# Kernel tuning notes

Measured on AMD Instinct MI355X. Metric: run time of the kernel, lower is better.

## Reference

```python
import jax, jax.numpy as jnp
import numpy as np

# Fixed varlen layout: 2 sequences of length 2048 packed into N=4096 tokens
B, S, H, HK, D = 2, 2048, 32, 8, 128
G = H // HK  # GQA group size
SCALE = 1.0 / float(np.sqrt(D))


def setup_inputs() -> dict:
    key = jax.random.key(0)
    k0, k1, k2 = jax.random.split(key, 3)
    N = B * S
    return {
        "q": jax.random.normal(k0, (N, H, D), jnp.float32),
        "k": jax.random.normal(k1, (N, HK, D), jnp.float32),
        "v": jax.random.normal(k2, (N, HK, D), jnp.float32),
        "k_cache": jnp.zeros((N, HK * D), jnp.float32),
        "v_cache": jnp.zeros((N, HK * D), jnp.float32),
        "slot_mapping": jnp.arange(N, dtype=jnp.int32),
    }


def reference(q, k, v, k_cache, v_cache, slot_mapping):
    N = q.shape[0]
    num_slots = k_cache.shape[0]
    # --- store_kvcache: scatter flattened K/V rows into paged slots; slot==-1 skipped ---
    safe = jnp.where(slot_mapping >= 0, slot_mapping, num_slots)  # out-of-range -> dropped
    k_cache_new = k_cache.at[safe].set(k.reshape(N, HK * D), mode="drop")
    v_cache_new = v_cache.at[safe].set(v.reshape(N, HK * D), mode="drop")
    # --- prefill path (block_tables=None): causal varlen attention on fresh k,v ---
    qb = q.reshape(B, S, HK, G, D)
    kb = k.reshape(B, S, HK, D)
    vb = v.reshape(B, S, HK, D)
    scores = jnp.einsum("bqhgd,bkhd->bhgqk", qb, kb) * SCALE  # [B,HK,G,S,S]
    causal = jnp.tril(jnp.ones((S, S), dtype=bool))
    scores = jnp.where(causal, scores, jnp.finfo(scores.dtype).min)
    p = jax.nn.softmax(scores, axis=-1)
    o = jnp.einsum("bhgqk,bkhd->bqhgd", p, vb).reshape(N, H, D)
    return o, k_cache_new, v_cache_new
```

## Files before the change

kernel.cpp:

```cpp
#include <hip/hip_runtime.h>
#include <stdint.h>
#include <math.h>

constexpr int B = 2, S = 2048, H = 32, HK = 8, D = 128;
constexpr int N = B * S;
constexpr int KVD = HK * D;
constexpr float SCALE = 0.08838834764831845f;
constexpr float LOG2E = 1.4426950408889634f;
constexpr float QSCALE = SCALE * LOG2E;

typedef __attribute__((ext_vector_type(8))) short short8;
typedef __attribute__((ext_vector_type(4))) float floatx4;

static __device__ __forceinline__ uint32_t f2bf1(float f) {
    union { float f; uint32_t u; } c; c.f = f;
    return (c.u + 0x7FFFu + ((c.u >> 16) & 1u)) >> 16;
}
static __device__ __forceinline__ uint32_t packbf(float a, float b) {
    return f2bf1(a) | (f2bf1(b) << 16);
}
static __device__ __forceinline__ uint32_t fbits(float f) {
    union { float f; uint32_t u; } c; c.f = f; return c.u;
}
static __device__ __forceinline__ uint32_t packtrunc(float lo, float hi) {
    return __builtin_amdgcn_perm(fbits(hi), fbits(lo), 0x07060302u);
}
static __device__ __forceinline__ void load_lds16(const void* g, void* l) {
    __builtin_amdgcn_global_load_lds((const __attribute__((address_space(1))) uint32_t*)g,
                                     (__attribute__((address_space(3))) uint32_t*)l,
                                     16, 0, 0);
}

__global__ __launch_bounds__(256) void k_prep(const float* __restrict__ k,
                                              const int* __restrict__ slot_mapping,
                                              float* __restrict__ kc_out,
                                              uint16_t* __restrict__ Kb) {
    int tid = blockIdx.x * 256 + threadIdx.x;
    int idx = tid * 4;
    int token = idx >> 10;
    int rem = idx & 1023;
    float4 val = *(const float4*)(k + idx);
    int s = slot_mapping[token];
    if (s >= 0 && s < N) {
        *(float4*)(kc_out + (size_t)s * KVD + rem) = val;
    }
    int b  = token >> 11;
    int ss = token & 2047;
    int hk = rem >> 7;
    int d  = rem & 127;
    uint2 pk;
    pk.x = packbf(val.x, val.y);
    pk.y = packbf(val.z, val.w);
    *(uint2*)(Kb + (((size_t)(b * HK + hk) * S + ss) * D + d)) = pk;
}

__global__ __launch_bounds__(256) void v_prep(const float* __restrict__ v,
                                              const int* __restrict__ slot_mapping,
                                              float* __restrict__ vc_out,
                                              uint16_t* __restrict__ Vt) {
    __shared__ float tile[64][129];
    int t = threadIdx.x;
    int kv0 = blockIdx.x * 64;
    int bhk = blockIdx.y;
    int b = bhk >> 3, hk = bhk & 7;

#pragma unroll
    for (int i = 0; i < 8; ++i) {
        int r = i * 8 + (t >> 5);
        int c = (t & 31) * 4;
        int token = b * S + kv0 + r;
        float4 val = *(const float4*)(v + (size_t)token * KVD + hk * D + c);
        int s = slot_mapping[token];
        if (s >= 0 && s < N) {
            *(float4*)(vc_out + (size_t)s * KVD + hk * D + c) = val;
        }
        tile[r][c + 0] = val.x; tile[r][c + 1] = val.y;
        tile[r][c + 2] = val.z; tile[r][c + 3] = val.w;
    }
    __syncthreads();
#pragma unroll
    for (int i = 0; i < 8; ++i) {
        int d = i * 16 + (t >> 4);
        int c = (t & 15) * 4;
        uint2 pk;
        pk.x = packbf(tile[c + 0][d], tile[c + 1][d]);
        pk.y = packbf(tile[c + 2][d], tile[c + 3][d]);
        *(uint2*)(Vt + ((size_t)(bhk * D + d)) * S + kv0 + c) = pk;
    }
}

__global__ __launch_bounds__(512, 2) void attn(const float* __restrict__ q,
                                               const uint16_t* __restrict__ Kb,
                                               const uint16_t* __restrict__ Vt,
                                               float* __restrict__ out) {
    __shared__ uint16_t sK[2][64 * 128];
    __shared__ uint16_t sV[2][128 * 64];

    int id = blockIdx.x;
    int hk = id & 7;
    int s0 = id >> 3;
    int x  = s0 & 7;
    int g2 = (s0 >> 3) & 1;
    int b  = s0 >> 4;
    int h0 = hk * 4 + g2 * 2;

    int t = threadIdx.x;
    int lane = t & 63, wave = t >> 6;
    int quad = lane >> 4, n = lane & 15, xr = n & 7;

    const uint16_t* Kbh = Kb + (size_t)(b * HK + hk) * S * D;
    const uint16_t* Vbh = Vt + (size_t)(b * HK + hk) * D * S;

    const uint16_t* gK[2]; const uint16_t* gV[2];
    int oK[2], oV[2];
#pragma unroll
    for (int j = 0; j < 2; ++j) {
        int i = wave * 2 + j;
        int rK = i * 4 + (lane >> 4);
        int cK = ((lane & 15) ^ (rK & 7)) * 8;
        gK[j] = Kbh + (size_t)rK * D + cK;
        oK[j] = i * 512;
        int rV = i * 8 + (lane >> 3);
        int cV = ((lane & 7) ^ (rV & 7)) * 8;
        gV[j] = Vbh + (size_t)rV * S + cV;
        oV[j] = i * 512;
    }

    for (int pass = 0; pass < 2; ++pass) {
        int qt = pass ? x : 15 - x;
        int q0 = qt * 128;
        int qwave = q0 + wave * 16;

        short8 bq[2][4];
#pragma unroll
        for (int g = 0; g < 2; ++g) {
            const float* qrow = q + (size_t)(b * S + qwave + n) * (H * D) + (h0 + g) * D + quad * 8;
#pragma unroll
            for (int kc = 0; kc < 4; ++kc) {
                float4 v0 = *(const float4*)(qrow + kc * 32);
                float4 v1 = *(const float4*)(qrow + kc * 32 + 4);
                uint4 pk;
                pk.x = packtrunc(v0.x * QSCALE, v0.y * QSCALE);
                pk.y = packtrunc(v0.z * QSCALE, v0.w * QSCALE);
                pk.z = packtrunc(v1.x * QSCALE, v1.y * QSCALE);
                pk.w = packtrunc(v1.z * QSCALE, v1.w * QSCALE);
                bq[g][kc] = *(short8*)&pk;
            }
        }

        floatx4 o_acc[2][8];
#pragma unroll
        for (int g = 0; g < 2; ++g)
#pragma unroll
            for (int i = 0; i < 8; ++i) o_acc[g][i] = (floatx4){0.f, 0.f, 0.f, 0.f};
        float lsum[2] = {0.f, 0.f};

        int nt = 2 * qt + 2;
        __syncthreads();
#pragma unroll
        for (int j = 0; j < 2; ++j) load_lds16(gK[j], &sK[0][0] + oK[j]);
#pragma unroll
        for (int j = 0; j < 2; ++j) load_lds16(gV[j], &sV[0][0] + oV[j]);

        for (int tile = 0; tile < nt; ++tile) {
            int cur = tile & 1;
            __syncthreads();
            if (tile + 1 < nt) {
                int kvn = (tile + 1) * 64;
#pragma unroll
                for (int j = 0; j < 2; ++j) load_lds16(gK[j] + (size_t)kvn * D, &sK[cur ^ 1][0] + oK[j]);
#pragma unroll
                for (int j = 0; j < 2; ++j) load_lds16(gV[j] + kvn, &sV[cur ^ 1][0] + oV[j]);
            }
            int kv0 = tile * 64;
            if (kv0 > qwave + 15) continue;

            const uint16_t* K_ = &sK[cur][0];
            const uint16_t* V_ = &sV[cur][0];

            floatx4 acc[2][4];
#pragma unroll
            for (int g = 0; g < 2; ++g)
#pragma unroll
                for (int sub = 0; sub < 4; ++sub) acc[g][sub] = (floatx4){0.f, 0.f, 0.f, 0.f};
#pragma unroll
            for (int sub = 0; sub < 4; ++sub) {
#pragma unroll
                for (int kc = 0; kc < 4; ++kc) {
                    short8 ak = *(const short8*)(K_ + (sub * 16 + n) * 128 + (((kc * 4 + quad) ^ xr) * 8));
                    acc[0][sub] = __builtin_amdgcn_mfma_f32_16x16x32_bf16(ak, bq[0][kc], acc[0][sub], 0, 0, 0);
                    acc[1][sub] = __builtin_amdgcn_mfma_f32_16x16x32_bf16(ak, bq[1][kc], acc[1][sub], 0, 0, 0);
                }
            }

            short8 ap[2][2];
            int qg = qwave + n;
            if (kv0 + 63 > qwave) {
#pragma unroll
                for (int sub = 0; sub < 4; ++sub)
#pragma unroll
                    for (int reg = 0; reg < 4; ++reg)
                        if (kv0 + sub * 16 + quad * 4 + reg > qg) {
                            acc[0][sub][reg] = -1e9f;
                            acc[1][sub][reg] = -1e9f;
                        }
            }
#pragma unroll
            for (int g = 0; g < 2; ++g) {
                float rs = 0.f;
                uint32_t pw[4][2];
#pragma unroll
                for (int sub = 0; sub < 4; ++sub) {
                    float p0 = __builtin_amdgcn_exp2f(acc[g][sub][0]);
                    float p1 = __builtin_amdgcn_exp2f(acc[g][sub][1]);
                    float p2 = __builtin_amdgcn_exp2f(acc[g][sub][2]);
                    float p3 = __builtin_amdgcn_exp2f(acc[g][sub][3]);
                    rs += (p0 + p1) + (p2 + p3);
                    pw[sub][0] = packtrunc(p0, p1);
                    pw[sub][1] = packtrunc(p2, p3);
                }
                lsum[g] += rs;

#pragma unroll
                for (int ks = 0; ks < 2; ++ks) {
                    uint32_t x0 = pw[2 * ks][0],     x1 = pw[2 * ks][1];
                    uint32_t y0 = pw[2 * ks + 1][0], y1 = pw[2 * ks + 1][1];
                    asm("v_permlane32_swap_b32 %0, %1" : "+v"(x0), "+v"(y0));
                    asm("v_permlane32_swap_b32 %0, %1" : "+v"(x1), "+v"(y1));
                    asm("v_permlane16_swap_b32 %0, %1" : "+v"(x0), "+v"(y0));
                    asm("v_permlane16_swap_b32 %0, %1" : "+v"(x1), "+v"(y1));
                    uint4 w; w.x = x0; w.y = x1; w.z = y0; w.w = y1;
                    ap[g][ks] = *(short8*)&w;
                }
            }

#pragma unroll
            for (int d8 = 0; d8 < 8; ++d8) {
#pragma unroll
                for (int ks = 0; ks < 2; ++ks) {
                    short8 bv = *(const short8*)(V_ + (d8 * 16 + n) * 64 + (((ks * 4 + quad) ^ xr) * 8));
                    o_acc[0][d8] = __builtin_amdgcn_mfma_f32_16x16x32_bf16(ap[0][ks], bv, o_acc[0][d8], 0, 0, 0);
                    o_acc[1][d8] = __builtin_amdgcn_mfma_f32_16x16x32_bf16(ap[1][ks], bv, o_acc[1][d8], 0, 0, 0);
                }
            }
        }

#pragma unroll
        for (int g = 0; g < 2; ++g) {
            float s = lsum[g];
            s += __shfl_xor(s, 16);
            s += __shfl_xor(s, 32);
            float linv = 1.0f / s;
            float lr[4];
#pragma unroll
            for (int reg = 0; reg < 4; ++reg) lr[reg] = __shfl(linv, quad * 4 + reg);
#pragma unroll
            for (int d8 = 0; d8 < 8; ++d8) {
#pragma unroll
                for (int reg = 0; reg < 4; ++reg) {
                    size_t row = (size_t)(b * S + qwave + quad * 4 + reg);
                    out[row * (H * D) + (h0 + g) * D + d8 * 16 + n] = o_acc[g][d8][reg] * lr[reg];
                }
            }
        }
    }
}

extern "C" void kernel_launch(void* const* d_in, const int* in_sizes, int n_in,
                              void* d_out, int out_size, void* d_ws, size_t ws_size,
                              hipStream_t stream) {
    const float* q = (const float*)d_in[0];
    const float* k = (const float*)d_in[1];
    const float* v = (const float*)d_in[2];
    const int* slot_mapping = (const int*)d_in[5];

    float* o_out  = (float*)d_out;
    float* kc_out = o_out + (size_t)N * H * D;
    float* vc_out = kc_out + (size_t)N * KVD;

    uint16_t* Kb = (uint16_t*)d_ws;
    uint16_t* Vt = Kb + (size_t)B * HK * S * D;

    k_prep<<<(N * KVD / 4) / 256, 256, 0, stream>>>(k, slot_mapping, kc_out, Kb);
    v_prep<<<dim3(S / 64, B * HK), 256, 0, stream>>>(v, slot_mapping, vc_out, Vt);
    attn<<<dim3(256), 512, 0, stream>>>(q, Kb, Vt, o_out);
}
```

Baseline: 262.2 us.

## Software-pipeline QK and softmax-PV across tiles with wave-staggered ordering

Splits the attention tile loop into separate QK and softmax+PV stages, then pipelines them so tile t's QK runs alongside tile t-1's softmax/PV. K and V staging are decoupled, and half the waves (by wave index) run PV before QK so the two halves issue different instruction mixes concurrently. The aim is to overlap exp/permute VALU work with MFMA work and to hide LDS load latency. In exchange it holds two score accumulator sets live, which raises register pressure at launch bounds 512x2, and it relies on the double-buffer indexing staying correct with one extra barrier.

```diff
diff --git a/kernel.cpp b/kernel.cpp
--- a/kernel.cpp
+++ b/kernel.cpp
@@ -107,6 +107,7 @@
     int t = threadIdx.x;
     int lane = t & 63, wave = t >> 6;
     int quad = lane >> 4, n = lane & 15, xr = n & 7;
+    bool pvFirst = (wave >> 2) & 1;
 
     const uint16_t* Kbh = Kb + (size_t)(b * HK + hk) * S * D;
     const uint16_t* Vbh = Vt + (size_t)(b * HK + hk) * D * S;
@@ -155,34 +156,24 @@
             for (int i = 0; i < 8; ++i) o_acc[g][i] = (floatx4){0.f, 0.f, 0.f, 0.f};
         float lsum[2] = {0.f, 0.f};
 
-        int nt = 2 * qt + 2;
-        __syncthreads();
-#pragma unroll
-        for (int j = 0; j < 2; ++j) load_lds16(gK[j], &sK[0][0] + oK[j]);
-#pragma unroll
-        for (int j = 0; j < 2; ++j) load_lds16(gV[j], &sV[0][0] + oV[j]);
-
-        for (int tile = 0; tile < nt; ++tile) {
-            int cur = tile & 1;
-            __syncthreads();
-            if (tile + 1 < nt) {
-                int kvn = (tile + 1) * 64;
-#pragma unroll
-                for (int j = 0; j < 2; ++j) load_lds16(gK[j] + (size_t)kvn * D, &sK[cur ^ 1][0] + oK[j]);
-#pragma unroll
-                for (int j = 0; j < 2; ++j) load_lds16(gV[j] + kvn, &sV[cur ^ 1][0] + oV[j]);
-            }
+        auto STAGE_K = [&](int tile) {
+            size_t kvn = (size_t)tile * 64;
+#pragma unroll
+            for (int j = 0; j < 2; ++j) load_lds16(gK[j] + kvn * D, &sK[tile & 1][0] + oK[j]);
+        };
+        auto STAGE_V = [&](int tile) {
+            size_t kvn = (size_t)tile * 64;
+#pragma unroll
+            for (int j = 0; j < 2; ++j) load_lds16(gV[j] + kvn, &sV[tile & 1][0] + oV[j]);
+        };
+        auto QK = [&](int tile, floatx4 (&acc)[2][4]) {
             int kv0 = tile * 64;
-            if (kv0 > qwave + 15) continue;
-
-            const uint16_t* K_ = &sK[cur][0];
-            const uint16_t* V_ = &sV[cur][0];
-
-            floatx4 acc[2][4];
 #pragma unroll
             for (int g = 0; g < 2; ++g)
 #pragma unroll
                 for (int sub = 0; sub < 4; ++sub) acc[g][sub] = (floatx4){0.f, 0.f, 0.f, 0.f};
+            if (kv0 > qwave + 15) return;
+            const uint16_t* K_ = &sK[tile & 1][0];
 #pragma unroll
             for (int sub = 0; sub < 4; ++sub) {
 #pragma unroll
@@ -192,8 +183,11 @@
                     acc[1][sub] = __builtin_amdgcn_mfma_f32_16x16x32_bf16(ak, bq[1][kc], acc[1][sub], 0, 0, 0);
                 }
             }
-
-            short8 ap[2][2];
+        };
+        auto SMPV = [&](int tile, floatx4 (&acc)[2][4]) {
+            int kv0 = tile * 64;
+            if (kv0 > qwave + 15) return;
+            const uint16_t* V_ = &sV[tile & 1][0];
             int qg = qwave + n;
             if (kv0 + 63 > qwave) {
 #pragma unroll
@@ -205,6 +199,7 @@
                             acc[1][sub][reg] = -1e9f;
                         }
             }
+            short8 ap[2][2];
 #pragma unroll
             for (int g = 0; g < 2; ++g) {
                 float rs = 0.f;
@@ -220,7 +215,6 @@
                     pw[sub][1] = packtrunc(p2, p3);
                 }
                 lsum[g] += rs;
-
 #pragma unroll
                 for (int ks = 0; ks < 2; ++ks) {
                     uint32_t x0 = pw[2 * ks][0],     x1 = pw[2 * ks][1];
@@ -233,7 +227,6 @@
                     ap[g][ks] = *(short8*)&w;
                 }
             }
-
 #pragma unroll
             for (int d8 = 0; d8 < 8; ++d8) {
 #pragma unroll
@@ -243,7 +236,39 @@
                     o_acc[1][d8] = __builtin_amdgcn_mfma_f32_16x16x32_bf16(ap[1][ks], bv, o_acc[1][d8], 0, 0, 0);
                 }
             }
+        };
+
+        int nt = 2 * qt + 2;
+        __syncthreads();
+        STAGE_K(0);
+
+        floatx4 accA[2][4], accB[2][4];
+
+        for (int tt = 0; tt < nt; tt += 2) {
+            __syncthreads();
+            if (tt + 1 < nt) STAGE_K(tt + 1);
+            STAGE_V(tt);
+            if (pvFirst) {
+                if (tt > 0) SMPV(tt - 1, accB);
+                QK(tt, accA);
+            } else {
+                QK(tt, accA);
+                if (tt > 0) SMPV(tt - 1, accB);
+            }
+
+            __syncthreads();
+            if (tt + 2 < nt) STAGE_K(tt + 2);
+            STAGE_V(tt + 1);
+            if (pvFirst) {
+                SMPV(tt, accA);
+                QK(tt + 1, accB);
+            } else {
+                QK(tt + 1, accB);
+                SMPV(tt, accA);
+            }
         }
+        __syncthreads();
+        SMPV(nt - 1, accB);
 
 #pragma unroll
         for (int g = 0; g < 2; ++g) {
```

Measured after the change: 260.7 us. About the same (-0.6%).
